# Kernel tuning notes

Hardware: AMD Instinct MI355X
Metric: run time of the kernel (lower is better)

Reference implementation:

```python
import jax, jax.numpy as jnp
import numpy as np

C_Z = 128
C_H = 128
N = 512
B = 1

def _layer_norm(x, g, b, eps=1e-5):
    mu = jnp.mean(x, axis=-1, keepdims=True)
    var = jnp.var(x, axis=-1, keepdims=True)
    return (x - mu) * jax.lax.rsqrt(var + eps) * g + b

def _linear(x, w, b):
    # torch Linear: y = x @ w.T + b, w: [out, in]
    return jnp.einsum('...i,oi->...o', x, w) + b

def setup_inputs() -> dict:
    key = jax.random.key(0)
    ks = jax.random.split(key, 8)
    s = 1.0 / np.sqrt(C_Z)
    return {
        'z': jax.random.normal(ks[0], (B, N, N, C_Z), jnp.float32),
        'mask': jnp.ones((B, N, N), jnp.float32),
        'ln_in_g': jnp.ones((C_Z,), jnp.float32),
        'ln_in_b': jnp.zeros((C_Z,), jnp.float32),
        'w_ag': jax.random.normal(ks[1], (C_H, C_Z), jnp.float32) * s,
        'b_ag': jnp.ones((C_H,), jnp.float32),
        'w_ap': jax.random.normal(ks[2], (C_H, C_Z), jnp.float32) * s,
        'b_ap': jnp.zeros((C_H,), jnp.float32),
        'w_bg': jax.random.normal(ks[3], (C_H, C_Z), jnp.float32) * s,
        'b_bg': jnp.ones((C_H,), jnp.float32),
        'w_bp': jax.random.normal(ks[4], (C_H, C_Z), jnp.float32) * s,
        'b_bp': jnp.zeros((C_H,), jnp.float32),
        'w_g': jax.random.normal(ks[5], (C_Z, C_Z), jnp.float32) * s,
        'b_g': jnp.zeros((C_Z,), jnp.float32),
        'w_z': jax.random.normal(ks[6], (C_Z, C_H), jnp.float32) * s,
        'b_z': jnp.zeros((C_Z,), jnp.float32),
        'ln_out_g': jnp.ones((C_H,), jnp.float32),
        'ln_out_b': jnp.zeros((C_H,), jnp.float32),
    }

def reference(z, mask, ln_in_g, ln_in_b, w_ag, b_ag, w_ap, b_ap,
              w_bg, b_bg, w_bp, b_bp, w_g, b_g, w_z, b_z,
              ln_out_g, ln_out_b):
    m = mask[..., None]                       # [B,N,N,1]
    zn = _layer_norm(z, ln_in_g, ln_in_b)     # [B,N,N,Cz]
    a = m * jax.nn.sigmoid(_linear(zn, w_ag, b_ag)) * _linear(zn, w_ap, b_ap)
    b = m * jax.nn.sigmoid(_linear(zn, w_bg, b_bg)) * _linear(zn, w_bp, b_bp)
    # outgoing: x[b,i,j,c] = sum_k a[b,i,k,c] * b[b,j,k,c]
    x = jnp.einsum('bikc,bjkc->bijc', a, b)
    x = _layer_norm(x, ln_out_g, ln_out_b)
    x = _linear(x, w_z, b_z)
    g = jax.nn.sigmoid(_linear(zn, w_g, b_g))
    return x * g
```

## Files before the change

kernel.cpp:

```cpp
#include <hip/hip_runtime.h>

#define NN 512
#define CCH 128
#define MM (NN*NN)

using f32x4  = __attribute__((ext_vector_type(4))) float;
using f32x2  = __attribute__((ext_vector_type(2))) float;
using bf16x8 = __attribute__((ext_vector_type(8))) short;
using u16x4  = __attribute__((ext_vector_type(4))) unsigned short;
using u32x2  = __attribute__((ext_vector_type(2))) unsigned int;
using u32x4  = __attribute__((ext_vector_type(4))) unsigned int;
typedef unsigned short u16;

__device__ __forceinline__ u16 f2bf(float f) {
    unsigned u = __builtin_bit_cast(unsigned, f);
    u += 0x7FFF + ((u >> 16) & 1);
    return (u16)(u >> 16);
}
__device__ __forceinline__ float bf2f(u16 h) {
    unsigned u = ((unsigned)h) << 16;
    return __builtin_bit_cast(float, u);
}
__device__ __forceinline__ unsigned pack2(float lo, float hi) {
    return (unsigned)f2bf(lo) | ((unsigned)f2bf(hi) << 16);
}
__device__ __forceinline__ float sigm(float x) { return 1.0f / (1.0f + __expf(-x)); }

__device__ __forceinline__ void gl_lds16(const void* g, void* l) {
    __builtin_amdgcn_global_load_lds(
        (const __attribute__((address_space(1))) void*)g,
        (__attribute__((address_space(3))) void*)l, 16, 0, 0);
}

__global__ __launch_bounds__(256) void k_prep(
    const float* __restrict__ w0, const float* __restrict__ w1,
    const float* __restrict__ w2, const float* __restrict__ w3,
    const float* __restrict__ w4, const float* __restrict__ w5,
    const float* __restrict__ b0, const float* __restrict__ b1,
    const float* __restrict__ b2, const float* __restrict__ b3,
    const float* __restrict__ b4, const float* __restrict__ b5,
    const float* __restrict__ gin, const float* __restrict__ bin,
    const float* __restrict__ gout, const float* __restrict__ bout,
    u16* __restrict__ wbf, float* __restrict__ bias2) {
    int mat = blockIdx.x;
    const float* W = mat==0?w0:mat==1?w1:mat==2?w2:mat==3?w3:mat==4?w4:w5;
    const float* B = mat==0?b0:mat==1?b1:mat==2?b2:mat==3?b3:mat==4?b4:b5;
    const float* G = (mat==5)? gout : gin;
    const float* Bt= (mat==5)? bout : bin;
    __shared__ float gs[CCH], bs[CCH];
    int tid = threadIdx.x;
    if (tid < CCH) { gs[tid] = G[tid]; bs[tid] = Bt[tid]; }
    __syncthreads();
    int o = tid >> 1, c0 = (tid & 1) * 64;
    const float* src = W + o * CCH + c0;
    char* dstrow = (char*)(wbf + mat * 16384) + o * 256;
    int key = o & 7;
    float dot = 0.f;
    #pragma unroll
    for (int q = 0; q < 16; ++q) {
        f32x4 v = *(const f32x4*)(src + q * 4);
        int c = c0 + q * 4;
        dot += bs[c]*v.x + bs[c+1]*v.y + bs[c+2]*v.z + bs[c+3]*v.w;
        u16x4 p;
        p.x = f2bf(v.x * gs[c]);     p.y = f2bf(v.y * gs[c+1]);
        p.z = f2bf(v.z * gs[c+2]);   p.w = f2bf(v.w * gs[c+3]);
        int chunk = (c0 >> 3) + (q >> 1);
        *(u16x4*)(dstrow + (((chunk ^ key)) << 4) + ((q & 1) << 3)) = p;
    }
    dot += __shfl_xor(dot, 1);
    if ((tid & 1) == 0) bias2[mat * CCH + o] = B[o] + dot;
}

__global__ __launch_bounds__(512, 4) void k_fused(
    const float* __restrict__ z, const float* __restrict__ mask,
    const u16* __restrict__ wbf, const float* __restrict__ bias2,
    u16* __restrict__ aT, u16* __restrict__ bT, u16* gateB) {
    __shared__ __align__(16) u16 wls[32768];
    int tid = threadIdx.x, w = tid >> 6, lane = tid & 63;
    int r = lane & 15, kq = lane >> 4;
    long m0 = (long)blockIdx.x * 128;

    {
        const char* Wg = (const char*)wbf;
        #pragma unroll
        for (int it = 0; it < 8; ++it)
            gl_lds16(Wg + (long)it * 8192 + tid * 16, (char*)wls + it * 8192 + w * 1024);
    }

    long mrow = m0 + w * 16 + r;
    bf16x8 av[4];
    {
        const float* zr = z + mrow * CCH;
        f32x4 zv[4][2];
        float s = 0.f, s2 = 0.f;
        #pragma unroll
        for (int kb = 0; kb < 4; ++kb) {
            zv[kb][0] = *(const f32x4*)(zr + kb * 32 + kq * 8);
            zv[kb][1] = *(const f32x4*)(zr + kb * 32 + kq * 8 + 4);
            #pragma unroll
            for (int h = 0; h < 2; ++h) {
                f32x4 v = zv[kb][h];
                s += v.x + v.y + v.z + v.w;
                s2 = fmaf(v.x, v.x, fmaf(v.y, v.y, fmaf(v.z, v.z, fmaf(v.w, v.w, s2))));
            }
        }
        s  += __shfl_xor(s, 16);  s  += __shfl_xor(s, 32);
        s2 += __shfl_xor(s2, 16); s2 += __shfl_xor(s2, 32);
        float mu = s * (1.0f / CCH);
        float var = fmaxf(s2 * (1.0f / CCH) - mu * mu, 0.f);
        float rs = rsqrtf(var + 1e-5f);
        #pragma unroll
        for (int kb = 0; kb < 4; ++kb) {
            f32x4 a0 = zv[kb][0], a1 = zv[kb][1];
            u32x4 o;
            o[0] = pack2((a0.x - mu) * rs, (a0.y - mu) * rs);
            o[1] = pack2((a0.z - mu) * rs, (a0.w - mu) * rs);
            o[2] = pack2((a1.x - mu) * rs, (a1.y - mu) * rs);
            o[3] = pack2((a1.z - mu) * rs, (a1.w - mu) * rs);
            av[kb] = __builtin_bit_cast(bf16x8, o);
        }
    }
    f32x4 mkv = *(const f32x4*)(mask + m0 + w * 16 + kq * 4);

    float b1v[4][2], b2v[4][2];
    #pragma unroll
    for (int nt = 0; nt < 8; ++nt) {
        b1v[nt >> 1][nt & 1] = bias2[0 * CCH + nt * 16 + r];
        b2v[nt >> 1][nt & 1] = bias2[1 * CCH + nt * 16 + r];
    }

    int i7 = (int)((blockIdx.x >> 2) & 7);
    int q = w * 2 + (kq >> 1);
    long boff = m0 * 2 + ((long)(q >> 3) << 7) + ((long)((q & 7) ^ i7) << 4)
              + ((kq & 1) << 3);

    __syncthreads();

    f32x4 acc1[8], acc2[8];
    #pragma unroll
    for (int nt = 0; nt < 8; ++nt) { acc1[nt] = {0,0,0,0}; acc2[nt] = {0,0,0,0}; }
    #pragma unroll
    for (int nt = 0; nt < 8; ++nt) {
        int ol = nt * 16 + r;
        int key = ol & 7;
        const char* row1 = (const char*)wls + ol * 256;
        const char* row2 = (const char*)wls + 32768 + ol * 256;
        #pragma unroll
        for (int kb = 0; kb < 4; ++kb) {
            int ph16 = ((kb * 4 + kq) ^ key) << 4;
            bf16x8 b1 = *(const bf16x8*)(row1 + ph16);
            bf16x8 b2 = *(const bf16x8*)(row2 + ph16);
            acc1[nt] = __builtin_amdgcn_mfma_f32_16x16x32_bf16(av[kb], b1, acc1[nt], 0, 0, 0);
            acc2[nt] = __builtin_amdgcn_mfma_f32_16x16x32_bf16(av[kb], b2, acc2[nt], 0, 0, 0);
        }
    }
    __syncthreads();

    {
        const char* Wg = (const char*)wbf + 65536;
        #pragma unroll
        for (int it = 0; it < 8; ++it)
            gl_lds16(Wg + (long)it * 8192 + tid * 16, (char*)wls + it * 8192 + w * 1024);
    }

    #pragma unroll
    for (int nt = 0; nt < 8; ++nt) {
        int cc = nt * 16 + r;
        float bb1 = b1v[nt >> 1][nt & 1], bb2 = b2v[nt >> 1][nt & 1];
        float v0 = mkv[0] * sigm(acc1[nt][0] + bb1) * (acc2[nt][0] + bb2);
        float v1 = mkv[1] * sigm(acc1[nt][1] + bb1) * (acc2[nt][1] + bb2);
        float v2 = mkv[2] * sigm(acc1[nt][2] + bb1) * (acc2[nt][2] + bb2);
        float v3 = mkv[3] * sigm(acc1[nt][3] + bb1) * (acc2[nt][3] + bb2);
        u32x2 pv; pv.x = pack2(v0, v1); pv.y = pack2(v2, v3);
        *(u32x2*)((char*)aT + ((long)cc << 19) + boff) = pv;
    }
    #pragma unroll
    for (int nt = 0; nt < 8; ++nt) {
        b1v[nt >> 1][nt & 1] = bias2[2 * CCH + nt * 16 + r];
        b2v[nt >> 1][nt & 1] = bias2[3 * CCH + nt * 16 + r];
    }
    __syncthreads();

    #pragma unroll
    for (int nt = 0; nt < 8; ++nt) { acc1[nt] = {0,0,0,0}; acc2[nt] = {0,0,0,0}; }
    #pragma unroll
    for (int nt = 0; nt < 8; ++nt) {
        int ol = nt * 16 + r;
        int key = ol & 7;
        const char* row1 = (const char*)wls + ol * 256;
        const char* row2 = (const char*)wls + 32768 + ol * 256;
        #pragma unroll
        for (int kb = 0; kb < 4; ++kb) {
            int ph16 = ((kb * 4 + kq) ^ key) << 4;
            bf16x8 b1 = *(const bf16x8*)(row1 + ph16);
            bf16x8 b2 = *(const bf16x8*)(row2 + ph16);
            acc1[nt] = __builtin_amdgcn_mfma_f32_16x16x32_bf16(av[kb], b1, acc1[nt], 0, 0, 0);
            acc2[nt] = __builtin_amdgcn_mfma_f32_16x16x32_bf16(av[kb], b2, acc2[nt], 0, 0, 0);
        }
    }
    __syncthreads();

    {
        const char* Wg = (const char*)wbf + 131072;
        #pragma unroll
        for (int it = 0; it < 4; ++it)
            gl_lds16(Wg + (long)it * 8192 + tid * 16, (char*)wls + it * 8192 + w * 1024);
    }

    #pragma unroll
    for (int nt = 0; nt < 8; ++nt) {
        int cc = nt * 16 + r;
        float bb1 = b1v[nt >> 1][nt & 1], bb2 = b2v[nt >> 1][nt & 1];
        float v0 = mkv[0] * sigm(acc1[nt][0] + bb1) * (acc2[nt][0] + bb2);
        float v1 = mkv[1] * sigm(acc1[nt][1] + bb1) * (acc2[nt][1] + bb2);
        float v2 = mkv[2] * sigm(acc1[nt][2] + bb1) * (acc2[nt][2] + bb2);
        float v3 = mkv[3] * sigm(acc1[nt][3] + bb1) * (acc2[nt][3] + bb2);
        u32x2 pv; pv.x = pack2(v0, v1); pv.y = pack2(v2, v3);
        *(u32x2*)((char*)bT + ((long)cc << 19) + boff) = pv;
    }
    f32x4 bg[8];
    #pragma unroll
    for (int nt = 0; nt < 8; ++nt)
        bg[nt] = *(const f32x4*)(bias2 + 4 * CCH + nt * 16 + kq * 4);
    __syncthreads();

    {
        f32x4 acc[8];
        #pragma unroll
        for (int nt = 0; nt < 8; ++nt) acc[nt] = {0,0,0,0};
        #pragma unroll
        for (int nt = 0; nt < 8; ++nt) {
            int ol = nt * 16 + r;
            int key = ol & 7;
            const char* row1 = (const char*)wls + ol * 256;
            #pragma unroll
            for (int kb = 0; kb < 4; ++kb) {
                bf16x8 b1 = *(const bf16x8*)(row1 + (((kb * 4 + kq) ^ key) << 4));
                acc[nt] = __builtin_amdgcn_mfma_f32_16x16x32_bf16(b1, av[kb], acc[nt], 0, 0, 0);
            }
        }
        #pragma unroll
        for (int nt = 0; nt < 8; ++nt) {
            int c0 = nt * 16 + kq * 4;
            u32x2 pv;
            pv.x = pack2(sigm(acc[nt][0] + bg[nt][0]), sigm(acc[nt][1] + bg[nt][1]));
            pv.y = pack2(sigm(acc[nt][2] + bg[nt][2]), sigm(acc[nt][3] + bg[nt][3]));
            *(u32x2*)(gateB + mrow * 256 + c0) = pv;
        }
    }
}

__global__ __launch_bounds__(256, 4) void k_tri(const u16* __restrict__ aT,
                                                const u16* __restrict__ bT,
                                                u16* __restrict__ xT) {
    __shared__ __align__(16) char shm[34816];
    u16* At = (u16*)shm;
    u16* Bt = (u16*)(shm + 16384);
    int tid = threadIdx.x;
    int w = tid >> 6, lane = tid & 63;
    int r = lane & 15, kq = lane >> 4;

    int L = blockIdx.x;
    int xcd = L & 7, idx = L >> 3;
    int c    = xcd + 8 * (idx >> 4);
    int tile = idx & 15;
    int ti = tile >> 2, tj = tile & 3;

    const char* abase = (const char*)(aT + (long)c * MM) + (long)(ti * 128) * 1024;
    const char* bbase = (const char*)(bT + (long)c * MM) + (long)(tj * 128) * 1024;
    int wm = w >> 1, wn = w & 1;

    f32x4 acc[4][4];
    #pragma unroll
    for (int a = 0; a < 4; ++a)
        #pragma unroll
        for (int bq = 0; bq < 4; ++bq) acc[a][bq] = {0.f,0.f,0.f,0.f};

    for (int ks = 0; ks < 8; ++ks) {
        const char* asrc = abase + ks * 128;
        const char* bsrc = bbase + ks * 128;
        #pragma unroll
        for (int it = 0; it < 4; ++it) {
            int u = it * 256 + tid;
            long goff = (long)(u >> 3) * 1024 + (u & 7) * 16;
            gl_lds16(asrc + goff, (char*)At + it * 4096 + w * 1024);
            gl_lds16(bsrc + goff, (char*)Bt + it * 4096 + w * 1024);
        }
        __syncthreads();

        #pragma unroll
        for (int kh = 0; kh < 2; ++kh) {
            bf16x8 af[4];
            #pragma unroll
            for (int mt = 0; mt < 4; ++mt) {
                int rowa = wm * 64 + mt * 16 + r;
                af[mt] = *(const bf16x8*)((const char*)At + rowa * 128 +
                                          (((kh * 4 + kq) ^ (r & 7)) << 4));
            }
            #pragma unroll
            for (int nt = 0; nt < 4; ++nt) {
                int rowb = wn * 64 + nt * 16 + r;
                bf16x8 bf = *(const bf16x8*)((const char*)Bt + rowb * 128 +
                                             (((kh * 4 + kq) ^ (r & 7)) << 4));
                #pragma unroll
                for (int mt = 0; mt < 4; ++mt)
                    acc[mt][nt] = __builtin_amdgcn_mfma_f32_16x16x32_bf16(bf, af[mt], acc[mt][nt], 0, 0, 0);
            }
        }
        __syncthreads();
    }

    char* tb = shm;
    #pragma unroll
    for (int mt = 0; mt < 4; ++mt) {
        int il = wm * 64 + mt * 16 + r;
        #pragma unroll
        for (int nt = 0; nt < 4; ++nt) {
            int jl = wn * 64 + nt * 16 + kq * 4;
            u32x2 pv;
            pv.x = pack2(acc[mt][nt][0], acc[mt][nt][1]);
            pv.y = pack2(acc[mt][nt][2], acc[mt][nt][3]);
            *(u32x2*)(tb + il * 272 + jl * 2) = pv;
        }
    }
    __syncthreads();
    u16* xrow = xT + (long)c * MM + (long)(ti * 128) * NN + tj * 128;
    int joff = tid & 15;
    #pragma unroll
    for (int rd = 0; rd < 8; ++rd) {
        int il = rd * 16 + (tid >> 4);
        u32x4 vv = *(const u32x4*)(tb + il * 272 + joff * 16);
        *(u32x4*)(xrow + (long)il * NN + joff * 8) = vv;
    }
}

__global__ __launch_bounds__(256, 4) void k_out(const u16* __restrict__ xT,
                                                const u16* __restrict__ wbf,
                                                const float* __restrict__ bias2,
                                                const u16* gateB,
                                                float* __restrict__ outp) {
    __shared__ __align__(16) u16 xl[64 * 128];
    int tid = threadIdx.x, w = tid >> 6, lane = tid & 63;
    int r = lane & 15, kq = lane >> 4;
    long m0 = (long)blockIdx.x * 64;

    {
        int cg = tid & 31, ms = tid >> 5;
        int c0 = cg * 4;
        const u16* base = xT + m0 + (long)ms * 8;
        bf16x8 v0 = *(const bf16x8*)(base + (long)(c0 + 0) * MM);
        bf16x8 v1 = *(const bf16x8*)(base + (long)(c0 + 1) * MM);
        bf16x8 v2 = *(const bf16x8*)(base + (long)(c0 + 2) * MM);
        bf16x8 v3 = *(const bf16x8*)(base + (long)(c0 + 3) * MM);
        #pragma unroll
        for (int e = 0; e < 8; ++e) {
            int m = ms * 8 + e;
            u16x4 t;
            t.x = (u16)v0[e]; t.y = (u16)v1[e]; t.z = (u16)v2[e]; t.w = (u16)v3[e];
            *(u16x4*)((char*)xl + m * 256 + ((c0 * 2) ^ ((m & 15) << 4))) = t;
        }
    }
    __syncthreads();

    int mlr = w * 16 + r;
    int swm = (mlr & 15) << 4;
    u32x4 avu[4];
    float s = 0.f, s2 = 0.f;
    #pragma unroll
    for (int kb = 0; kb < 4; ++kb) {
        avu[kb] = *(const u32x4*)((const char*)xl + mlr * 256 + ((kb * 64 + kq * 16) ^ swm));
        #pragma unroll
        for (int p = 0; p < 4; ++p) {
            unsigned u = avu[kb][p];
            float flo = __builtin_bit_cast(float, u << 16);
            float fhi = __builtin_bit_cast(float, u & 0xFFFF0000u);
            s += flo + fhi;
            s2 = fmaf(flo, flo, s2);
            s2 = fmaf(fhi, fhi, s2);
        }
    }
    s  += __shfl_xor(s, 16);  s  += __shfl_xor(s, 32);
    s2 += __shfl_xor(s2, 16); s2 += __shfl_xor(s2, 32);
    float mu = s * (1.0f / CCH);
    float var = fmaxf(s2 * (1.0f / CCH) - mu * mu, 0.f);
    float rs = rsqrtf(var + 1e-5f);
    float nmu = -mu * rs;
    bf16x8 av[4];
    #pragma unroll
    for (int kb = 0; kb < 4; ++kb) {
        u32x4 o;
        #pragma unroll
        for (int p = 0; p < 4; ++p) {
            unsigned u = avu[kb][p];
            float flo = __builtin_bit_cast(float, u << 16);
            float fhi = __builtin_bit_cast(float, u & 0xFFFF0000u);
            o[p] = pack2(fmaf(flo, rs, nmu), fmaf(fhi, rs, nmu));
        }
        av[kb] = __builtin_bit_cast(bf16x8, o);
    }

    long m = m0 + w * 16 + r;
    u16x4 gvu[8];
    f32x4 bb[8];
    #pragma unroll
    for (int nt = 0; nt < 8; ++nt) {
        gvu[nt] = *(const u16x4*)(gateB + m * 256 + nt * 16 + kq * 4);
        bb[nt]  = *(const f32x4*)(bias2 + 5 * CCH + nt * 16 + kq * 4);
    }

    const char* Wz = (const char*)(wbf + 5 * 16384);
    f32x4 acc[8];
    #pragma unroll
    for (int nt = 0; nt < 8; ++nt) acc[nt] = {0,0,0,0};
    #pragma unroll
    for (int nt = 0; nt < 8; ++nt) {
        int ol = nt * 16 + r;
        int key = ol & 7;
        const char* row = Wz + ol * 256;
        #pragma unroll
        for (int kb = 0; kb < 4; ++kb) {
            bf16x8 bw = *(const bf16x8*)(row + (((kb * 4 + kq) ^ key) << 4));
            acc[nt] = __builtin_amdgcn_mfma_f32_16x16x32_bf16(bw, av[kb], acc[nt], 0, 0, 0);
        }
    }

    __syncthreads();

    #pragma unroll
    for (int nt = 0; nt < 8; ++nt) {
        int c0 = nt * 16 + kq * 4;
        f32x4 o;
        #pragma unroll
        for (int j = 0; j < 4; ++j)
            o[j] = (acc[nt][j] + bb[nt][j]) * bf2f(gvu[nt][j]);
        *(f32x4*)(outp + m * CCH + c0) = o;
    }
}

extern "C" void kernel_launch(void* const* d_in, const int* in_sizes, int n_in,
                              void* d_out, int out_size, void* d_ws, size_t ws_size,
                              hipStream_t stream) {
    const float* z       = (const float*)d_in[0];
    const float* mask    = (const float*)d_in[1];
    const float* ln_in_g = (const float*)d_in[2];
    const float* ln_in_b = (const float*)d_in[3];
    const float* w_ag    = (const float*)d_in[4];
    const float* b_ag    = (const float*)d_in[5];
    const float* w_ap    = (const float*)d_in[6];
    const float* b_ap    = (const float*)d_in[7];
    const float* w_bg    = (const float*)d_in[8];
    const float* b_bg    = (const float*)d_in[9];
    const float* w_bp    = (const float*)d_in[10];
    const float* b_bp    = (const float*)d_in[11];
    const float* w_g     = (const float*)d_in[12];
    const float* b_g     = (const float*)d_in[13];
    const float* w_z     = (const float*)d_in[14];
    const float* b_z     = (const float*)d_in[15];
    const float* ln_o_g  = (const float*)d_in[16];
    const float* ln_o_b  = (const float*)d_in[17];
    float* out = (float*)d_out;
    u16* gateB = (u16*)d_out;

    char* ws = (char*)d_ws;
    const size_t SL = (size_t)MM * CCH * 2;
    u16* xT   = (u16*)ws;
    u16* aT   = (u16*)(ws + SL);
    u16* bT   = (u16*)(ws + 2 * SL);
    u16* wbf  = (u16*)(ws + 3 * SL);
    float* b2 = (float*)(ws + 3 * SL + 6 * 16384 * 2);

    k_prep<<<6, 256, 0, stream>>>(w_ag, w_ap, w_bg, w_bp, w_g, w_z,
                                  b_ag, b_ap, b_bg, b_bp, b_g, b_z,
                                  ln_in_g, ln_in_b, ln_o_g, ln_o_b, wbf, b2);
    k_fused<<<MM / 128, 512, 0, stream>>>(z, mask, wbf, b2, aT, bT, gateB);
    k_tri<<<2048, 256, 0, stream>>>(aT, bT, xT);
    k_out<<<MM / 64, 256, 0, stream>>>(xT, wbf, b2, gateB, out);
}
```

Baseline: 291.7 us.

## Switch intermediates and MFMAs from bf16 to fp16 and stage output through LDS

Converts all bf16 weights, activations and intermediates to fp16 and uses the fp16 MFMA instruction in place of the bf16 one. The final output stage now goes through a padded LDS tile so that global float stores are written as contiguous rows. The transposed x load is also rewritten from vector loads into scalar element loads. fp16 gives finer mantissa precision but a narrower range, so the triangle einsum products and sums could overflow or lose accuracy.

```diff
diff --git a/kernel.cpp b/kernel.cpp
--- a/kernel.cpp
+++ b/kernel.cpp
@@ -6,23 +6,20 @@
 
 using f32x4  = __attribute__((ext_vector_type(4))) float;
 using f32x2  = __attribute__((ext_vector_type(2))) float;
-using bf16x8 = __attribute__((ext_vector_type(8))) short;
+using f16x8  = __attribute__((ext_vector_type(8))) _Float16;
 using u16x4  = __attribute__((ext_vector_type(4))) unsigned short;
 using u32x2  = __attribute__((ext_vector_type(2))) unsigned int;
 using u32x4  = __attribute__((ext_vector_type(4))) unsigned int;
 typedef unsigned short u16;
 
-__device__ __forceinline__ u16 f2bf(float f) {
-    unsigned u = __builtin_bit_cast(unsigned, f);
-    u += 0x7FFF + ((u >> 16) & 1);
-    return (u16)(u >> 16);
-}
-__device__ __forceinline__ float bf2f(u16 h) {
-    unsigned u = ((unsigned)h) << 16;
-    return __builtin_bit_cast(float, u);
+__device__ __forceinline__ u16 f2h(float f) {
+    return __builtin_bit_cast(u16, (_Float16)f);
+}
+__device__ __forceinline__ float h2f(u16 h) {
+    return (float)__builtin_bit_cast(_Float16, h);
 }
 __device__ __forceinline__ unsigned pack2(float lo, float hi) {
-    return (unsigned)f2bf(lo) | ((unsigned)f2bf(hi) << 16);
+    return (unsigned)f2h(lo) | ((unsigned)f2h(hi) << 16);
 }
 __device__ __forceinline__ float sigm(float x) { return 1.0f / (1.0f + __expf(-x)); }
 
@@ -62,8 +59,8 @@
         int c = c0 + q * 4;
         dot += bs[c]*v.x + bs[c+1]*v.y + bs[c+2]*v.z + bs[c+3]*v.w;
         u16x4 p;
-        p.x = f2bf(v.x * gs[c]);     p.y = f2bf(v.y * gs[c+1]);
-        p.z = f2bf(v.z * gs[c+2]);   p.w = f2bf(v.w * gs[c+3]);
+        p.x = f2h(v.x * gs[c]);     p.y = f2h(v.y * gs[c+1]);
+        p.z = f2h(v.z * gs[c+2]);   p.w = f2h(v.w * gs[c+3]);
         int chunk = (c0 >> 3) + (q >> 1);
         *(u16x4*)(dstrow + (((chunk ^ key)) << 4) + ((q & 1) << 3)) = p;
     }
@@ -88,7 +85,7 @@
     }
 
     long mrow = m0 + w * 16 + r;
-    bf16x8 av[4];
+    f16x8 av[4];
     {
         const float* zr = z + mrow * CCH;
         f32x4 zv[4][2];
@@ -117,7 +114,7 @@
             o[1] = pack2((a0.z - mu) * rs, (a0.w - mu) * rs);
             o[2] = pack2((a1.x - mu) * rs, (a1.y - mu) * rs);
             o[3] = pack2((a1.z - mu) * rs, (a1.w - mu) * rs);
-            av[kb] = __builtin_bit_cast(bf16x8, o);
+            av[kb] = __builtin_bit_cast(f16x8, o);
         }
     }
     f32x4 mkv = *(const f32x4*)(mask + m0 + w * 16 + kq * 4);
@@ -148,10 +145,10 @@
         #pragma unroll
         for (int kb = 0; kb < 4; ++kb) {
             int ph16 = ((kb * 4 + kq) ^ key) << 4;
-            bf16x8 b1 = *(const bf16x8*)(row1 + ph16);
-            bf16x8 b2 = *(const bf16x8*)(row2 + ph16);
-            acc1[nt] = __builtin_amdgcn_mfma_f32_16x16x32_bf16(av[kb], b1, acc1[nt], 0, 0, 0);
-            acc2[nt] = __builtin_amdgcn_mfma_f32_16x16x32_bf16(av[kb], b2, acc2[nt], 0, 0, 0);
+            f16x8 b1 = *(const f16x8*)(row1 + ph16);
+            f16x8 b2 = *(const f16x8*)(row2 + ph16);
+            acc1[nt] = __builtin_amdgcn_mfma_f32_16x16x32_f16(av[kb], b1, acc1[nt], 0, 0, 0);
+            acc2[nt] = __builtin_amdgcn_mfma_f32_16x16x32_f16(av[kb], b2, acc2[nt], 0, 0, 0);
         }
     }
     __syncthreads();
@@ -192,10 +189,10 @@
         #pragma unroll
         for (int kb = 0; kb < 4; ++kb) {
             int ph16 = ((kb * 4 + kq) ^ key) << 4;
-            bf16x8 b1 = *(const bf16x8*)(row1 + ph16);
-            bf16x8 b2 = *(const bf16x8*)(row2 + ph16);
-            acc1[nt] = __builtin_amdgcn_mfma_f32_16x16x32_bf16(av[kb], b1, acc1[nt], 0, 0, 0);
-            acc2[nt] = __builtin_amdgcn_mfma_f32_16x16x32_bf16(av[kb], b2, acc2[nt], 0, 0, 0);
+            f16x8 b1 = *(const f16x8*)(row1 + ph16);
+            f16x8 b2 = *(const f16x8*)(row2 + ph16);
+            acc1[nt] = __builtin_amdgcn_mfma_f32_16x16x32_f16(av[kb], b1, acc1[nt], 0, 0, 0);
+            acc2[nt] = __builtin_amdgcn_mfma_f32_16x16x32_f16(av[kb], b2, acc2[nt], 0, 0, 0);
         }
     }
     __syncthreads();
@@ -235,8 +232,8 @@
             const char* row1 = (const char*)wls + ol * 256;
             #pragma unroll
             for (int kb = 0; kb < 4; ++kb) {
-                bf16x8 b1 = *(const bf16x8*)(row1 + (((kb * 4 + kq) ^ key) << 4));
-                acc[nt] = __builtin_amdgcn_mfma_f32_16x16x32_bf16(b1, av[kb], acc[nt], 0, 0, 0);
+                f16x8 b1 = *(const f16x8*)(row1 + (((kb * 4 + kq) ^ key) << 4));
+                acc[nt] = __builtin_amdgcn_mfma_f32_16x16x32_f16(b1, av[kb], acc[nt], 0, 0, 0);
             }
         }
         #pragma unroll
@@ -290,21 +287,21 @@
 
         #pragma unroll
         for (int kh = 0; kh < 2; ++kh) {
-            bf16x8 af[4];
+            f16x8 af[4];
             #pragma unroll
             for (int mt = 0; mt < 4; ++mt) {
                 int rowa = wm * 64 + mt * 16 + r;
-                af[mt] = *(const bf16x8*)((const char*)At + rowa * 128 +
-                                          (((kh * 4 + kq) ^ (r & 7)) << 4));
+                af[mt] = *(const f16x8*)((const char*)At + rowa * 128 +
+                                         (((kh * 4 + kq) ^ (r & 7)) << 4));
             }
             #pragma unroll
             for (int nt = 0; nt < 4; ++nt) {
                 int rowb = wn * 64 + nt * 16 + r;
-                bf16x8 bf = *(const bf16x8*)((const char*)Bt + rowb * 128 +
-                                             (((kh * 4 + kq) ^ (r & 7)) << 4));
+                f16x8 bf = *(const f16x8*)((const char*)Bt + rowb * 128 +
+                                           (((kh * 4 + kq) ^ (r & 7)) << 4));
                 #pragma unroll
                 for (int mt = 0; mt < 4; ++mt)
-                    acc[mt][nt] = __builtin_amdgcn_mfma_f32_16x16x32_bf16(bf, af[mt], acc[mt][nt], 0, 0, 0);
+                    acc[mt][nt] = __builtin_amdgcn_mfma_f32_16x16x32_f16(bf, af[mt], acc[mt][nt], 0, 0, 0);
             }
         }
         __syncthreads();
@@ -339,7 +336,8 @@
                                                 const float* __restrict__ bias2,
                                                 const u16* gateB,
                                                 float* __restrict__ outp) {
-    __shared__ __align__(16) u16 xl[64 * 128];
+    __shared__ __align__(16) char shm[34816];
+    u16* xl = (u16*)shm;
     int tid = threadIdx.x, w = tid >> 6, lane = tid & 63;
     int r = lane & 15, kq = lane >> 4;
     long m0 = (long)blockIdx.x * 64;
@@ -348,15 +346,15 @@
         int cg = tid & 31, ms = tid >> 5;
         int c0 = cg * 4;
         const u16* base = xT + m0 + (long)ms * 8;
-        bf16x8 v0 = *(const bf16x8*)(base + (long)(c0 + 0) * MM);
-        bf16x8 v1 = *(const bf16x8*)(base + (long)(c0 + 1) * MM);
-        bf16x8 v2 = *(const bf16x8*)(base + (long)(c0 + 2) * MM);
-        bf16x8 v3 = *(const bf16x8*)(base + (long)(c0 + 3) * MM);
+        u16x4 t;
+        const u16* s0 = base + (long)(c0 + 0) * MM;
+        const u16* s1 = base + (long)(c0 + 1) * MM;
+        const u16* s2 = base + (long)(c0 + 2) * MM;
+        const u16* s3 = base + (long)(c0 + 3) * MM;
         #pragma unroll
         for (int e = 0; e < 8; ++e) {
             int m = ms * 8 + e;
-            u16x4 t;
-            t.x = (u16)v0[e]; t.y = (u16)v1[e]; t.z = (u16)v2[e]; t.w = (u16)v3[e];
+            t.x = s0[e]; t.y = s1[e]; t.z = s2[e]; t.w = s3[e];
             *(u16x4*)((char*)xl + m * 256 + ((c0 * 2) ^ ((m & 15) << 4))) = t;
         }
     }
@@ -372,8 +370,8 @@
         #pragma unroll
         for (int p = 0; p < 4; ++p) {
             unsigned u = avu[kb][p];
-            float flo = __builtin_bit_cast(float, u << 16);
-            float fhi = __builtin_bit_cast(float, u & 0xFFFF0000u);
+            float flo = h2f((u16)(u & 0xFFFFu));
+            float fhi = h2f((u16)(u >> 16));
             s += flo + fhi;
             s2 = fmaf(flo, flo, s2);
             s2 = fmaf(fhi, fhi, s2);
@@ -385,18 +383,18 @@
     float var = fmaxf(s2 * (1.0f / CCH) - mu * mu, 0.f);
     float rs = rsqrtf(var + 1e-5f);
     float nmu = -mu * rs;
-    bf16x8 av[4];
+    f16x8 av[4];
     #pragma unroll
     for (int kb = 0; kb < 4; ++kb) {
         u32x4 o;
         #pragma unroll
         for (int p = 0; p < 4; ++p) {
             unsigned u = avu[kb][p];
-            float flo = __builtin_bit_cast(float, u << 16);
-            float fhi = __builtin_bit_cast(float, u & 0xFFFF0000u);
+            float flo = h2f((u16)(u & 0xFFFFu));
+            float fhi = h2f((u16)(u >> 16));
             o[p] = pack2(fmaf(flo, rs, nmu), fmaf(fhi, rs, nmu));
         }
-        av[kb] = __builtin_bit_cast(bf16x8, o);
+        av[kb] = __builtin_bit_cast(f16x8, o);
     }
 
     long m = m0 + w * 16 + r;
@@ -419,21 +417,37 @@
         const char* row = Wz + ol * 256;
         #pragma unroll
         for (int kb = 0; kb < 4; ++kb) {
-            bf16x8 bw = *(const bf16x8*)(row + (((kb * 4 + kq) ^ key) << 4));
-            acc[nt] = __builtin_amdgcn_mfma_f32_16x16x32_bf16(bw, av[kb], acc[nt], 0, 0, 0);
-        }
-    }
-
-    __syncthreads();
-
-    #pragma unroll
-    for (int nt = 0; nt < 8; ++nt) {
-        int c0 = nt * 16 + kq * 4;
-        f32x4 o;
-        #pragma unroll
-        for (int j = 0; j < 4; ++j)
-            o[j] = (acc[nt][j] + bb[nt][j]) * bf2f(gvu[nt][j]);
-        *(f32x4*)(outp + m * CCH + c0) = o;
+            f16x8 bw = *(const f16x8*)(row + (((kb * 4 + kq) ^ key) << 4));
+            acc[nt] = __builtin_amdgcn_mfma_f32_16x16x32_f16(bw, av[kb], acc[nt], 0, 0, 0);
+        }
+    }
+
+    __syncthreads();
+
+    {
+        char* tile = shm;
+        int ml = w * 16 + r;
+        #pragma unroll
+        for (int nt = 0; nt < 8; ++nt) {
+            int c0 = nt * 16 + kq * 4;
+            f32x4 o;
+            #pragma unroll
+            for (int j = 0; j < 4; ++j)
+                o[j] = (acc[nt][j] + bb[nt][j]) * h2f(gvu[nt][j]);
+            *(f32x4*)(tile + ml * 528 + c0 * 4) = o;
+        }
+    }
+    __syncthreads();
+
+    {
+        const char* tile = shm;
+        int part = tid & 31;
+        #pragma unroll
+        for (int rd = 0; rd < 8; ++rd) {
+            int ml = rd * 8 + (tid >> 5);
+            f32x4 v = *(const f32x4*)(tile + ml * 528 + part * 16);
+            *(f32x4*)(outp + (m0 + ml) * CCH + part * 4) = v;
+        }
     }
 }
 
```

After: 286.4 us. About the same (-1.8%).
